# Kernel optimization log

Measured on AMD Instinct MI355X. Metric: run time of the kernel, lower is better.

## Reference

```python
import jax, jax.numpy as jnp
import numpy as np

Q_MAX = 127.0  # symmetric int8 range

def setup_inputs() -> dict:
    key = jax.random.key(0)
    k1, k2, k3, k4 = jax.random.split(key, 4)
    B, S, K, N = 4, 2048, 4096, 4096
    inp = jax.random.normal(k1, (B, S, K), dtype=jnp.float32)
    # int8 weight in [-127, 127], stored via randint(0,255)-127 per spec
    qweight = (jax.random.randint(k2, (N, K), 0, 255) - 127).astype(jnp.int8)
    # per-out-channel weight dequant scales (small positive)
    wparams = (jax.random.uniform(k3, (N,), dtype=jnp.float32) * 0.02 + 0.001)
    bias = jax.random.normal(k4, (N,), dtype=jnp.float32) * 0.1
    return {"inp": inp, "qweight": qweight, "wparams": wparams, "bias": bias}

def reference(inp, qweight, wparams, bias):
    # inp: [B, S, K] float32; qweight: [N, K] int8; wparams: [N]; bias: [N]
    B, S, K = inp.shape
    x = inp.reshape(B * S, K)
    # qntz: per-row symmetric absmax quantization of the activation to int8
    a_scale = jnp.max(jnp.abs(x), axis=1, keepdims=True) / Q_MAX  # [M, 1]
    qinp = jnp.clip(jnp.round(x / a_scale), -Q_MAX, Q_MAX).astype(jnp.int8)  # [M, K]
    d = jax.lax.dot_general(qinp, qweight.T, (((1,), (0,)), ((), ())),
                            preferred_element_type=jnp.int32)  # [M, N]
    # dqntz: scale by per-row act scale and per-col weight scale, add bias
    out = d.astype(jnp.float32) * a_scale * wparams[None, :] + bias[None, :]
    return out.reshape(B, S, -1)
```

## Files before the change

### kernel.cpp

```cpp
#include <hip/hip_runtime.h>
#include <hip/hip_bf16.h>


using int32x4 = __attribute__((ext_vector_type(4))) int;

#define QMAXF 127.0f

__global__ __launch_bounds__(256) void repack_weights(
    const int* __restrict__ w, signed char* __restrict__ w8, int total)
{
    bool is32 = true;
#pragma unroll
    for (int i = 0; i < 16; ++i) {
        int v = w[i];
        is32 = is32 && (v >= -127 && v <= 127);
    }

    const int t = blockIdx.x * blockDim.x + threadIdx.x;
    const int nth = gridDim.x * blockDim.x;
    const int chunks = total / 16;

    if (is32) {
        for (int c = t; c < chunks; c += nth) {
            const int32x4* src = reinterpret_cast<const int32x4*>(w + (size_t)c * 16);
            int32x4 a0 = src[0], a1 = src[1], a2 = src[2], a3 = src[3];
            int32x4 o;
            o[0] = (a0[0] & 0xff) | ((a0[1] & 0xff) << 8) | ((a0[2] & 0xff) << 16) | ((a0[3] & 0xff) << 24);
            o[1] = (a1[0] & 0xff) | ((a1[1] & 0xff) << 8) | ((a1[2] & 0xff) << 16) | ((a1[3] & 0xff) << 24);
            o[2] = (a2[0] & 0xff) | ((a2[1] & 0xff) << 8) | ((a2[2] & 0xff) << 16) | ((a2[3] & 0xff) << 24);
            o[3] = (a3[0] & 0xff) | ((a3[1] & 0xff) << 8) | ((a3[2] & 0xff) << 16) | ((a3[3] & 0xff) << 24);
            reinterpret_cast<int32x4*>(w8)[c] = o;
        }
    } else {
        const int32x4* src = reinterpret_cast<const int32x4*>(w);
        int32x4* dst = reinterpret_cast<int32x4*>(w8);
        for (int c = t; c < chunks; c += nth) dst[c] = src[c];
    }
}

__global__ __launch_bounds__(256) void quant_rows(
    const float* __restrict__ x, signed char* __restrict__ q,
    float* __restrict__ scale, int K)
{
    const int row = blockIdx.x;
    const int t = threadIdx.x;
    const float4* xr = reinterpret_cast<const float4*>(x + (size_t)row * K);

    float4 v[4];
    float m = 0.f;
#pragma unroll
    for (int i = 0; i < 4; ++i) {
        v[i] = xr[t + i * 256];
        m = fmaxf(m, fmaxf(fmaxf(fabsf(v[i].x), fabsf(v[i].y)),
                           fmaxf(fabsf(v[i].z), fabsf(v[i].w))));
    }
#pragma unroll
    for (int off = 32; off >= 1; off >>= 1)
        m = fmaxf(m, __shfl_xor(m, off, 64));
    __shared__ float wmax[4];
    const int wave = t >> 6;
    if ((t & 63) == 0) wmax[wave] = m;
    __syncthreads();
    m = fmaxf(fmaxf(wmax[0], wmax[1]), fmaxf(wmax[2], wmax[3]));

    const float s   = m / QMAXF;
    const float inv = (m > 0.f) ? (QMAXF / m) : 0.f;
    if (t == 0) scale[row] = s;

    int* qr = reinterpret_cast<int*>(q + (size_t)row * K);
#pragma unroll
    for (int i = 0; i < 4; ++i) {
        const float* f = reinterpret_cast<const float*>(&v[i]);
        unsigned int packed = 0;
#pragma unroll
        for (int j = 0; j < 4; ++j) {
            int qi = __float2int_rn(f[j] * inv);
            qi = qi > 127 ? 127 : (qi < -127 ? -127 : qi);
            packed |= ((unsigned int)(qi & 0xff)) << (8 * j);
        }
        qr[t + i * 256] = (int)packed;
    }
}

#define BM 256
#define BN 256
#define BKB 64
#define NBUF 4

__device__ __forceinline__ void async_copy16(const void* g, void* lds) {
    __builtin_amdgcn_global_load_lds(
        (const __attribute__((address_space(1))) void*)g,
        (__attribute__((address_space(3))) void*)lds, 16, 0, 0);
}

__global__ __launch_bounds__(512, 2) void gemm_i8_dequant_8ph(
    const signed char* __restrict__ A,
    const signed char* __restrict__ B,
    const float* __restrict__ a_scale,
    const float* __restrict__ wparams,
    const float* __restrict__ bias,
    float* __restrict__ out,
    int M, int N, int K)
{
    __shared__ __align__(16) signed char lds[NBUF * 32768];

    const int t    = threadIdx.x;
    const int lane = t & 63;
    const int wave = t >> 6;
    const int wr   = wave >> 2;
    const int wc   = wave & 3;

    const int nwg = gridDim.x;
    const int cpx = nwg >> 3;
    const int swz = (blockIdx.x & 7) * cpx + (blockIdx.x >> 3);
    const int nbx = N / BN;
    const int rowBase = (swz / nbx) * BM;
    const int colBase = (swz % nbx) * BN;

    const int r15 = lane & 15;
    const int ksl = lane >> 4;

    int32x4 acc[8][4] = {};
    const int NT = K / BKB;

    const signed char* gA0 = A + (size_t)(rowBase + wave * 16 + r15)       * K + ksl * 16;
    const signed char* gA1 = A + (size_t)(rowBase + (8 + wave) * 16 + r15) * K + ksl * 16;
    const signed char* gB0 = B + (size_t)(colBase + wave * 16 + r15)       * K + ksl * 16;
    const signed char* gB1 = B + (size_t)(colBase + (8 + wave) * 16 + r15) * K + ksl * 16;

    auto stageA = [&](int kt, int d) {
        signed char* L = lds + d * 32768;
        async_copy16(gA0 + kt, L + wave * 1024);
        async_copy16(gA1 + kt, L + (8 + wave) * 1024);
    };
    auto stageB = [&](int kt, int d) {
        signed char* L = lds + d * 32768 + 16384;
        async_copy16(gB0 + kt, L + wave * 1024);
        async_copy16(gB1 + kt, L + (8 + wave) * 1024);
    };

    auto computeTile = [&](int d, int tn, bool doStage) {
        const signed char* Ab = lds + d * 32768;
        const signed char* Bb = Ab + 16384;
        const int dn = tn & (NBUF - 1);

        if (doStage) stageA(tn * BKB, dn);
        int32x4 af[8], bf[4];
#pragma unroll
        for (int mm = 0; mm < 4; ++mm)
            af[mm] = *reinterpret_cast<const int32x4*>(
                Ab + (wr * 8 + mm) * 1024 + lane * 16);
#pragma unroll
        for (int nn = 0; nn < 4; ++nn)
            bf[nn] = *reinterpret_cast<const int32x4*>(
                Bb + (wc * 4 + nn) * 1024 + lane * 16);
        __builtin_amdgcn_s_setprio(1);
#pragma unroll
        for (int mm = 0; mm < 4; ++mm)
#pragma unroll
            for (int nn = 0; nn < 4; ++nn)
                acc[mm][nn] = __builtin_amdgcn_mfma_i32_16x16x64_i8(
                    af[mm], bf[nn], acc[mm][nn], 0, 0, 0);
        __builtin_amdgcn_s_setprio(0);

        if (doStage) stageB(tn * BKB, dn);
#pragma unroll
        for (int mm = 4; mm < 8; ++mm)
            af[mm] = *reinterpret_cast<const int32x4*>(
                Ab + (wr * 8 + mm) * 1024 + lane * 16);
        __builtin_amdgcn_s_setprio(1);
#pragma unroll
        for (int mm = 4; mm < 8; ++mm)
#pragma unroll
            for (int nn = 0; nn < 4; ++nn)
                acc[mm][nn] = __builtin_amdgcn_mfma_i32_16x16x64_i8(
                    af[mm], bf[nn], acc[mm][nn], 0, 0, 0);
        __builtin_amdgcn_s_setprio(0);
    };

    stageA(0, 0);        stageB(0, 0);
    stageA(BKB, 1);      stageB(BKB, 1);
    stageA(2 * BKB, 2);  stageB(2 * BKB, 2);
    asm volatile("s_waitcnt vmcnt(8)" ::: "memory");
    __builtin_amdgcn_s_barrier();

    for (int tt = 0; tt <= NT - 4; ++tt) {
        computeTile(tt & (NBUF - 1), tt + 3, true);
        asm volatile("s_waitcnt vmcnt(8)" ::: "memory");
        __builtin_amdgcn_s_barrier();
    }
    computeTile((NT - 3) & (NBUF - 1), 0, false);
    asm volatile("s_waitcnt vmcnt(4)" ::: "memory");
    __builtin_amdgcn_s_barrier();
    computeTile((NT - 2) & (NBUF - 1), 0, false);
    asm volatile("s_waitcnt vmcnt(0)" ::: "memory");
    __builtin_amdgcn_s_barrier();
    computeTile((NT - 1) & (NBUF - 1), 0, false);

#pragma unroll
    for (int mm = 0; mm < 8; ++mm) {
        const int rb = rowBase + wr * 128 + mm * 16 + ksl * 4;
        float asc[4];
#pragma unroll
        for (int r = 0; r < 4; ++r) asc[r] = a_scale[rb + r];
#pragma unroll
        for (int nn = 0; nn < 4; ++nn) {
            const int col = colBase + wc * 64 + nn * 16 + r15;
            const float wp = wparams[col];
            const float bs = bias[col];
#pragma unroll
            for (int r = 0; r < 4; ++r) {
                out[(size_t)(rb + r) * N + col] =
                    (float)acc[mm][nn][r] * asc[r] * wp + bs;
            }
        }
    }
}

extern "C" void kernel_launch(void* const* d_in, const int* in_sizes, int n_in,
                              void* d_out, int out_size, void* d_ws, size_t ws_size,
                              hipStream_t stream) {
    const float* inp     = (const float*)d_in[0];
    const int*   qw_raw  = (const int*)d_in[1];
    const float* wparams = (const float*)d_in[2];
    const float* bias    = (const float*)d_in[3];
    float*       out     = (float*)d_out;

    const int N = in_sizes[2];
    const int K = in_sizes[1] / N;
    const int M = in_sizes[0] / K;

    signed char* qinp    = (signed char*)d_ws;
    float*       a_scale = (float*)((char*)d_ws + (size_t)M * K);
    size_t off_w8 = (size_t)M * K + (((size_t)M * sizeof(float) + 255) & ~(size_t)255);
    signed char* w8      = (signed char*)((char*)d_ws + off_w8);

    repack_weights<<<2048, 256, 0, stream>>>(qw_raw, w8, N * K);
    quant_rows<<<M, 256, 0, stream>>>(inp, qinp, a_scale, K);

    const int nwg = (M / BM) * (N / BN);
    gemm_i8_dequant_8ph<<<nwg, 512, 0, stream>>>(
        qinp, w8, a_scale, wparams, bias, out, M, N, K);
}
```

Baseline: 203.4 us.

## Double-buffer LDS fragments in registers to overlap LDS reads with MFMA

Restructures the GEMM main loop so each wave loads the next K-tile's A/B fragments from LDS into a second register set while issuing MFMAs on the current set. Global-to-LDS prefetch now runs four tiles deep with tile-indexed buffer selection. The loop is unrolled by two with ping-pong register arrays and an explicit epilogue. This hides LDS read latency behind matrix math, at the cost of about 96 extra VGPRs for fragments, which may pressure the 2-wave occupancy target.

```diff
diff --git a/kernel.cpp b/kernel.cpp
--- a/kernel.cpp
+++ b/kernel.cpp
@@ -93,7 +93,7 @@
         (__attribute__((address_space(3))) void*)lds, 16, 0, 0);
 }
 
-__global__ __launch_bounds__(512, 2) void gemm_i8_dequant_8ph(
+__global__ __launch_bounds__(512, 2) void gemm_i8_dequant_rp(
     const signed char* __restrict__ A,
     const signed char* __restrict__ B,
     const float* __restrict__ a_scale,
@@ -128,74 +128,80 @@
     const signed char* gB0 = B + (size_t)(colBase + wave * 16 + r15)       * K + ksl * 16;
     const signed char* gB1 = B + (size_t)(colBase + (8 + wave) * 16 + r15) * K + ksl * 16;
 
-    auto stageA = [&](int kt, int d) {
-        signed char* L = lds + d * 32768;
+    auto stageA = [&](int tile) {
+        signed char* L = lds + (tile & (NBUF - 1)) * 32768;
+        const size_t kt = (size_t)tile * BKB;
         async_copy16(gA0 + kt, L + wave * 1024);
         async_copy16(gA1 + kt, L + (8 + wave) * 1024);
     };
-    auto stageB = [&](int kt, int d) {
-        signed char* L = lds + d * 32768 + 16384;
+    auto stageB = [&](int tile) {
+        signed char* L = lds + (tile & (NBUF - 1)) * 32768 + 16384;
+        const size_t kt = (size_t)tile * BKB;
         async_copy16(gB0 + kt, L + wave * 1024);
         async_copy16(gB1 + kt, L + (8 + wave) * 1024);
     };
-
-    auto computeTile = [&](int d, int tn, bool doStage) {
-        const signed char* Ab = lds + d * 32768;
+    auto ldFrags = [&](int tile, int32x4 (&fa)[8], int32x4 (&fb)[4]) {
+        const signed char* Ab = lds + (tile & (NBUF - 1)) * 32768;
         const signed char* Bb = Ab + 16384;
-        const int dn = tn & (NBUF - 1);
-
-        if (doStage) stageA(tn * BKB, dn);
-        int32x4 af[8], bf[4];
-#pragma unroll
-        for (int mm = 0; mm < 4; ++mm)
-            af[mm] = *reinterpret_cast<const int32x4*>(
+#pragma unroll
+        for (int mm = 0; mm < 8; ++mm)
+            fa[mm] = *reinterpret_cast<const int32x4*>(
                 Ab + (wr * 8 + mm) * 1024 + lane * 16);
 #pragma unroll
         for (int nn = 0; nn < 4; ++nn)
-            bf[nn] = *reinterpret_cast<const int32x4*>(
+            fb[nn] = *reinterpret_cast<const int32x4*>(
                 Bb + (wc * 4 + nn) * 1024 + lane * 16);
+    };
+    auto mfmaAll = [&](const int32x4 (&fa)[8], const int32x4 (&fb)[4]) {
         __builtin_amdgcn_s_setprio(1);
 #pragma unroll
-        for (int mm = 0; mm < 4; ++mm)
+        for (int mm = 0; mm < 8; ++mm)
 #pragma unroll
             for (int nn = 0; nn < 4; ++nn)
                 acc[mm][nn] = __builtin_amdgcn_mfma_i32_16x16x64_i8(
-                    af[mm], bf[nn], acc[mm][nn], 0, 0, 0);
+                    fa[mm], fb[nn], acc[mm][nn], 0, 0, 0);
         __builtin_amdgcn_s_setprio(0);
-
-        if (doStage) stageB(tn * BKB, dn);
-#pragma unroll
-        for (int mm = 4; mm < 8; ++mm)
-            af[mm] = *reinterpret_cast<const int32x4*>(
-                Ab + (wr * 8 + mm) * 1024 + lane * 16);
-        __builtin_amdgcn_s_setprio(1);
-#pragma unroll
-        for (int mm = 4; mm < 8; ++mm)
-#pragma unroll
-            for (int nn = 0; nn < 4; ++nn)
-                acc[mm][nn] = __builtin_amdgcn_mfma_i32_16x16x64_i8(
-                    af[mm], bf[nn], acc[mm][nn], 0, 0, 0);
-        __builtin_amdgcn_s_setprio(0);
-    };
-
-    stageA(0, 0);        stageB(0, 0);
-    stageA(BKB, 1);      stageB(BKB, 1);
-    stageA(2 * BKB, 2);  stageB(2 * BKB, 2);
+    };
+
+    int32x4 rA0[8], rB0[4], rA1[8], rB1[4];
+
+    stageA(0); stageB(0);
+    stageA(1); stageB(1);
+    stageA(2); stageB(2);
+    stageA(3); stageB(3);
     asm volatile("s_waitcnt vmcnt(8)" ::: "memory");
     __builtin_amdgcn_s_barrier();
-
-    for (int tt = 0; tt <= NT - 4; ++tt) {
-        computeTile(tt & (NBUF - 1), tt + 3, true);
-        asm volatile("s_waitcnt vmcnt(8)" ::: "memory");
+    ldFrags(0, rA0, rB0);
+    asm volatile("s_waitcnt lgkmcnt(0)" ::: "memory");
+    __builtin_amdgcn_s_barrier();
+
+    for (int tt = 0; tt < NT - 4; tt += 2) {
+        stageA(tt + 4);
+        ldFrags(tt + 1, rA1, rB1);
+        stageB(tt + 4);
+        mfmaAll(rA0, rB0);
+        asm volatile("s_waitcnt vmcnt(8) lgkmcnt(0)" ::: "memory");
         __builtin_amdgcn_s_barrier();
-    }
-    computeTile((NT - 3) & (NBUF - 1), 0, false);
-    asm volatile("s_waitcnt vmcnt(4)" ::: "memory");
-    __builtin_amdgcn_s_barrier();
-    computeTile((NT - 2) & (NBUF - 1), 0, false);
-    asm volatile("s_waitcnt vmcnt(0)" ::: "memory");
-    __builtin_amdgcn_s_barrier();
-    computeTile((NT - 1) & (NBUF - 1), 0, false);
+
+        stageA(tt + 5);
+        ldFrags(tt + 2, rA0, rB0);
+        stageB(tt + 5);
+        mfmaAll(rA1, rB1);
+        asm volatile("s_waitcnt vmcnt(8) lgkmcnt(0)" ::: "memory");
+        __builtin_amdgcn_s_barrier();
+    }
+
+    ldFrags(NT - 3, rA1, rB1);
+    mfmaAll(rA0, rB0);
+    asm volatile("s_waitcnt vmcnt(4) lgkmcnt(0)" ::: "memory");
+    __builtin_amdgcn_s_barrier();
+    ldFrags(NT - 2, rA0, rB0);
+    mfmaAll(rA1, rB1);
+    asm volatile("s_waitcnt vmcnt(0) lgkmcnt(0)" ::: "memory");
+    __builtin_amdgcn_s_barrier();
+    ldFrags(NT - 1, rA1, rB1);
+    mfmaAll(rA0, rB0);
+    mfmaAll(rA1, rB1);
 
 #pragma unroll
     for (int mm = 0; mm < 8; ++mm) {
@@ -239,6 +245,6 @@
     quant_rows<<<M, 256, 0, stream>>>(inp, qinp, a_scale, K);
 
     const int nwg = (M / BM) * (N / BN);
-    gemm_i8_dequant_8ph<<<nwg, 512, 0, stream>>>(
+    gemm_i8_dequant_rp<<<nwg, 512, 0, stream>>>(
         qinp, w8, a_scale, wparams, bias, out, M, N, K);
 }
```

Result: no change. 203.7 us (+0.2%).
